# Kernel optimization log

Measured on AMD Instinct MI355X. Metric: run time of the kernel, lower is better.

## Reference

```python
import math
import jax, jax.numpy as jnp
import numpy as np

B, S, D = 8, 2048, 512
D_MODEL = 512

def setup_inputs() -> dict:
    key = jax.random.key(0)
    kq, kk, kv = jax.random.split(key, 3)
    return {
        "query": jax.random.normal(kq, (B, S, D), dtype=jnp.float32),
        "key":   jax.random.normal(kk, (B, S, D), dtype=jnp.float32),
        "value": jax.random.normal(kv, (B, S, D), dtype=jnp.float32),
    }

def reference(query, key, value):
    # scores: [B, S, S]
    scores = jnp.einsum("bqd,bkd->bqk", query, key) / math.sqrt(D_MODEL)
    k = max(1, int(scores.shape[-1] * 0.1))
    top_scores, top_idx = jax.lax.top_k(scores, k)  # [B, S, k]
    # scatter top-k scores into a zero matrix (non-topk entries stay 0,
    # and DO participate in the softmax, matching the torch code)
    b_idx = jnp.arange(scores.shape[0])[:, None, None]
    q_idx = jnp.arange(scores.shape[1])[None, :, None]
    sparse = jnp.zeros_like(scores).at[b_idx, q_idx, top_idx].set(top_scores)
    attn = jax.nn.softmax(sparse, axis=-1)
    return jnp.einsum("bqk,bkd->bqd", attn, value)
```

## Files before the change

kernel.cpp:

```cpp
#include <hip/hip_runtime.h>
#include <math.h>

#define B_ 8
#define S_ 2048
#define D_ 512
#define KTOP 204
#define QK_SCALE 0.044194173824159216f

typedef short bfrag8 __attribute__((ext_vector_type(8)));
typedef float facc4 __attribute__((ext_vector_type(4)));

__device__ __forceinline__ unsigned short f2bf(float f) {
  unsigned u = __float_as_uint(f);
  u += 0x7FFFu + ((u >> 16) & 1);
  return (unsigned short)(u >> 16);
}

__device__ __forceinline__ unsigned fkey(float f) {
  unsigned b = __float_as_uint(f);
  return (b & 0x80000000u) ? ~b : (b | 0x80000000u);
}
__device__ __forceinline__ float keyfloat(unsigned k) {
  unsigned b = (k & 0x80000000u) ? (k & 0x7FFFFFFFu) : ~k;
  return __uint_as_float(b);
}

__device__ __forceinline__ void load16(const unsigned short* g, unsigned short* l) {
  __builtin_amdgcn_global_load_lds(
      (const __attribute__((address_space(1))) void*)g,
      (__attribute__((address_space(3))) void*)l, 16, 0, 0);
}

__global__ __launch_bounds__(256) void cvt_qk(const float* __restrict__ Q,
                                              const float* __restrict__ K,
                                              unsigned short* __restrict__ Qb,
                                              unsigned short* __restrict__ Kb) {
  const float* in = blockIdx.y ? K : Q;
  unsigned short* out = blockIdx.y ? Kb : Qb;
  int i = (blockIdx.x * 256 + threadIdx.x) * 4;
  float4 v = *(const float4*)(in + i);
  ushort4 o;
  o.x = f2bf(v.x); o.y = f2bf(v.y); o.z = f2bf(v.z); o.w = f2bf(v.w);
  *(ushort4*)(out + i) = o;
}

__global__ __launch_bounds__(256) void transpose_v(const float* __restrict__ V,
                                                   unsigned short* __restrict__ VT) {
  __shared__ float tile[32][33];
  int b = blockIdx.z;
  int d0 = blockIdx.x * 32, k0 = blockIdx.y * 32;
  const float* Vb = V + (size_t)b * S_ * D_;
  unsigned short* VTb = VT + (size_t)b * D_ * S_;
  int c = threadIdx.x & 31, r = threadIdx.x >> 5;
#pragma unroll
  for (int rr = 0; rr < 32; rr += 8)
    tile[r + rr][c] = Vb[(size_t)(k0 + r + rr) * D_ + d0 + c];
  __syncthreads();
#pragma unroll
  for (int rr = 0; rr < 32; rr += 8)
    VTb[(size_t)(d0 + r + rr) * S_ + k0 + c] = f2bf(tile[c][r + rr]);
}

__global__ __launch_bounds__(256) void gemm_qk(
    const unsigned short* __restrict__ A, int lda, long long astr,
    const unsigned short* __restrict__ Bm, int ldb, long long bstr,
    float* __restrict__ C, int ldc, long long cstr,
    int kdim, float scale) {
  const unsigned j = blockIdx.x + 16u * blockIdx.y + 256u * blockIdx.z;
  const unsigned bz = j & 7u;
  const unsigned q = j >> 3;
  const unsigned by = q & 15u;
  const unsigned bx = q >> 4;

  __shared__ unsigned short smA[128 * 32];
  __shared__ unsigned short smB[128 * 32];
  const int tid = threadIdx.x;
  const int wave = tid >> 6, lane = tid & 63;
  const int quad = lane >> 4, l15 = lane & 15;
  const unsigned short* Ab = A + (long long)bz * astr + (size_t)(by * 128) * lda;
  const unsigned short* Bb = Bm + (long long)bz * bstr + (size_t)(bx * 128) * ldb;
  const int srow = tid >> 2;
  const int scol = (tid & 3) * 8;
  unsigned short* lA0 = smA + wave * 512;
  unsigned short* lA1 = smA + 2048 + wave * 512;
  unsigned short* lB0 = smB + wave * 512;
  unsigned short* lB1 = smB + 2048 + wave * 512;
  const int mrow = 64 * (wave >> 1);
  const int nrow = 64 * (wave & 1);

  facc4 acc[4][4];
  const facc4 fzero = {0.f, 0.f, 0.f, 0.f};
#pragma unroll
  for (int i = 0; i < 4; ++i)
#pragma unroll
    for (int j2 = 0; j2 < 4; ++j2) acc[i][j2] = fzero;

  for (int k0 = 0; k0 < kdim; k0 += 32) {
    __syncthreads();
    load16(Ab + (size_t)srow * lda + k0 + scol, lA0);
    load16(Ab + (size_t)(srow + 64) * lda + k0 + scol, lA1);
    load16(Bb + (size_t)srow * ldb + k0 + scol, lB0);
    load16(Bb + (size_t)(srow + 64) * ldb + k0 + scol, lB1);
    __syncthreads();
    bfrag8 af[4], bq[4];
#pragma unroll
    for (int i = 0; i < 4; ++i)
      af[i] = *(const bfrag8*)(smA + (mrow + 16 * i + l15) * 32 + quad * 8);
#pragma unroll
    for (int j2 = 0; j2 < 4; ++j2)
      bq[j2] = *(const bfrag8*)(smB + (nrow + 16 * j2 + l15) * 32 + quad * 8);
#pragma unroll
    for (int i = 0; i < 4; ++i)
#pragma unroll
      for (int j2 = 0; j2 < 4; ++j2)
        acc[i][j2] = __builtin_amdgcn_mfma_f32_16x16x32_bf16(af[i], bq[j2], acc[i][j2], 0, 0, 0);
  }

  float* Cb = C + (long long)bz * cstr;
  const int mg = by * 128 + mrow;
  const int ng = bx * 128 + nrow;
#pragma unroll
  for (int i = 0; i < 4; ++i)
#pragma unroll
    for (int j2 = 0; j2 < 4; ++j2)
#pragma unroll
      for (int r = 0; r < 4; ++r)
        Cb[(size_t)(mg + 16 * i + quad * 4 + r) * ldc + ng + 16 * j2 + l15] = acc[i][j2][r] * scale;
}

__global__ __launch_bounds__(256) void gemm_pv(
    const unsigned short* __restrict__ A, int lda, long long astr,
    const unsigned short* __restrict__ Bm, int ldb, long long bstr,
    float* __restrict__ C, int ldc, long long cstr,
    int kdim, float scale) {
  const unsigned j = blockIdx.x + 4u * blockIdx.y + 64u * blockIdx.z;
  const unsigned bz = j & 7u;
  const unsigned q = j >> 3;
  const unsigned bx = q & 3u;
  const unsigned by = q >> 2;

  __shared__ unsigned short smA[128 * 32];
  __shared__ unsigned short smB[128 * 32];
  const int tid = threadIdx.x;
  const int wave = tid >> 6, lane = tid & 63;
  const int quad = lane >> 4, l15 = lane & 15;
  const unsigned short* Ab = A + (long long)bz * astr + (size_t)(by * 128) * lda;
  const unsigned short* Bb = Bm + (long long)bz * bstr + (size_t)(bx * 128) * ldb;
  const int srow = tid >> 2;
  const int scol = (tid & 3) * 8;
  unsigned short* lA0 = smA + wave * 512;
  unsigned short* lA1 = smA + 2048 + wave * 512;
  unsigned short* lB0 = smB + wave * 512;
  unsigned short* lB1 = smB + 2048 + wave * 512;
  const int mrow = 64 * (wave >> 1);
  const int nrow = 64 * (wave & 1);

  facc4 acc[4][4];
  const facc4 fzero = {0.f, 0.f, 0.f, 0.f};
#pragma unroll
  for (int i = 0; i < 4; ++i)
#pragma unroll
    for (int j2 = 0; j2 < 4; ++j2) acc[i][j2] = fzero;

  for (int k0 = 0; k0 < kdim; k0 += 32) {
    __syncthreads();
    load16(Ab + (size_t)srow * lda + k0 + scol, lA0);
    load16(Ab + (size_t)(srow + 64) * lda + k0 + scol, lA1);
    load16(Bb + (size_t)srow * ldb + k0 + scol, lB0);
    load16(Bb + (size_t)(srow + 64) * ldb + k0 + scol, lB1);
    __syncthreads();
    bfrag8 af[4], bq[4];
#pragma unroll
    for (int i = 0; i < 4; ++i)
      af[i] = *(const bfrag8*)(smA + (mrow + 16 * i + l15) * 32 + quad * 8);
#pragma unroll
    for (int j2 = 0; j2 < 4; ++j2)
      bq[j2] = *(const bfrag8*)(smB + (nrow + 16 * j2 + l15) * 32 + quad * 8);
#pragma unroll
    for (int i = 0; i < 4; ++i)
#pragma unroll
      for (int j2 = 0; j2 < 4; ++j2)
        acc[i][j2] = __builtin_amdgcn_mfma_f32_16x16x32_bf16(af[i], bq[j2], acc[i][j2], 0, 0, 0);
  }

  float* Cb = C + (long long)bz * cstr;
  const int mg = by * 128 + mrow;
  const int ng = bx * 128 + nrow;
#pragma unroll
  for (int i = 0; i < 4; ++i)
#pragma unroll
    for (int j2 = 0; j2 < 4; ++j2)
#pragma unroll
      for (int r = 0; r < 4; ++r)
        Cb[(size_t)(mg + 16 * i + quad * 4 + r) * ldc + ng + 16 * j2 + l15] = acc[i][j2][r] * scale;
}

__global__ __launch_bounds__(256) void topk_softmax(float* __restrict__ scores) {
  __shared__ unsigned binsAll[4][256];
  const int tid = threadIdx.x;
  const int wave = tid >> 6, lane = tid & 63;
  const long long row = (long long)blockIdx.x * 4 + wave;
  float* srow = scores + row * 2048;
  unsigned* bins = binsAll[wave];

  unsigned k[32];
#pragma unroll
  for (int c = 0; c < 4; ++c) {
    float4 a = *(const float4*)(srow + c * 512 + lane * 8);
    float4 b = *(const float4*)(srow + c * 512 + lane * 8 + 4);
    k[c * 8 + 0] = fkey(a.x); k[c * 8 + 1] = fkey(a.y);
    k[c * 8 + 2] = fkey(a.z); k[c * 8 + 3] = fkey(a.w);
    k[c * 8 + 4] = fkey(b.x); k[c * 8 + 5] = fkey(b.y);
    k[c * 8 + 6] = fkey(b.z); k[c * 8 + 7] = fkey(b.w);
  }

  unsigned kmax = 0;
#pragma unroll
  for (int i = 0; i < 32; ++i) kmax = max(kmax, k[i]);
#pragma unroll
  for (int off = 1; off < 64; off <<= 1)
    kmax = max(kmax, (unsigned)__shfl_xor((int)kmax, off));
  const float m = fmaxf(keyfloat(kmax), 0.f);

  unsigned prefix = 0, mmask = 0, krem = KTOP;
  for (int shift = 24; shift >= 0; shift -= 8) {
    uint4 z; z.x = z.y = z.z = z.w = 0;
    *(uint4*)(bins + lane * 4) = z;
#pragma unroll
    for (int i = 0; i < 32; ++i)
      if ((k[i] & mmask) == prefix) atomicAdd(&bins[(k[i] >> shift) & 255], 1u);
    uint4 b = *(const uint4*)(bins + lane * 4);
    unsigned s = b.x + b.y + b.z + b.w;
    unsigned t = s;
#pragma unroll
    for (int off = 1; off < 64; off <<= 1) {
      unsigned u = (unsigned)__shfl_down((int)t, off);
      t += (lane + off < 64) ? u : 0u;
    }
    const unsigned texcl = t - s;
    const unsigned c3 = texcl + b.w;
    const unsigned c2 = c3 + b.z;
    const unsigned c1 = c2 + b.y;
    const unsigned c0 = c1 + b.x;
    unsigned pack = 0;
    if (c0 >= krem && c1 < krem)   pack = ((krem - c1) << 8) | (lane * 4 + 0);
    if (c1 >= krem && c2 < krem)   pack = ((krem - c2) << 8) | (lane * 4 + 1);
    if (c2 >= krem && c3 < krem)   pack = ((krem - c3) << 8) | (lane * 4 + 2);
    if (c3 >= krem && texcl < krem) pack = ((krem - texcl) << 8) | (lane * 4 + 3);
#pragma unroll
    for (int off = 1; off < 64; off <<= 1)
      pack |= (unsigned)__shfl_xor((int)pack, off);
    prefix |= (pack & 255u) << shift;
    krem = pack >> 8;
    mmask |= 0xFFu << shift;
  }
  const unsigned tkey = prefix;

  unsigned cut;
  {
    unsigned tiem = 0;
#pragma unroll
    for (int i = 0; i < 32; ++i)
      if (k[i] == tkey) tiem |= 1u << i;
    unsigned need = krem;
    for (;;) {
      unsigned myidx = 0xFFFFFFFFu;
      if (tiem) {
        int i = __ffs((int)tiem) - 1;
        myidx = ((unsigned)(i >> 3)) * 512u + (unsigned)lane * 8u + (unsigned)(i & 7);
      }
      unsigned minidx = myidx;
#pragma unroll
      for (int off = 1; off < 64; off <<= 1)
        minidx = min(minidx, (unsigned)__shfl_xor((int)minidx, off));
      if (--need == 0 || minidx == 0xFFFFFFFFu) { cut = minidx; break; }
      if (myidx == minidx) tiem &= tiem - 1;
    }
  }

  const float eqw = __expf(keyfloat(tkey) - m);
  const float base = __expf(-m);
  float zsum = 0.f;
#pragma unroll
  for (int i = 0; i < 32; ++i) {
    const unsigned key = k[i];
    const unsigned idx = ((unsigned)(i >> 3)) * 512u + (unsigned)lane * 8u + (unsigned)(i & 7);
    float w;
    if (key > tkey) w = __expf(keyfloat(key) - m);
    else w = (key == tkey && idx <= cut) ? eqw : base;
    zsum += w;
    k[i] = __float_as_uint(w);
  }
#pragma unroll
  for (int off = 1; off < 64; off <<= 1) zsum += __shfl_xor(zsum, off);
  const float invZ = 1.f / zsum;

  unsigned short* arow = (unsigned short*)scores + row * 4096;
#pragma unroll
  for (int c = 0; c < 4; ++c) {
    union { unsigned short u[8]; int4 v4; } pk;
#pragma unroll
    for (int j = 0; j < 8; ++j)
      pk.u[j] = f2bf(__uint_as_float(k[c * 8 + j]) * invZ);
    *(int4*)(arow + c * 512 + lane * 8) = pk.v4;
  }
}

extern "C" void kernel_launch(void* const* d_in, const int* in_sizes, int n_in,
                              void* d_out, int out_size, void* d_ws, size_t ws_size,
                              hipStream_t stream) {
  const float* Q = (const float*)d_in[0];
  const float* K = (const float*)d_in[1];
  const float* V = (const float*)d_in[2];
  float* out = (float*)d_out;
  char* ws = (char*)d_ws;
  unsigned short* Qb = (unsigned short*)(ws);
  unsigned short* Kb = (unsigned short*)(ws + ((size_t)16 << 20));
  unsigned short* VT = (unsigned short*)(ws + ((size_t)32 << 20));
  float* scores = (float*)(ws + ((size_t)48 << 20));

  const int nel = B_ * S_ * D_;
  cvt_qk<<<dim3(nel / 1024, 2), 256, 0, stream>>>(Q, K, Qb, Kb);
  transpose_v<<<dim3(D_ / 32, S_ / 32, B_), 256, 0, stream>>>(V, VT);
  gemm_qk<<<dim3(S_ / 128, S_ / 128, B_), 256, 0, stream>>>(
      Qb, D_, (long long)S_ * D_, Kb, D_, (long long)S_ * D_,
      scores, S_, (long long)S_ * S_, D_, QK_SCALE);
  topk_softmax<<<B_ * S_ / 4, 256, 0, stream>>>(scores);
  gemm_pv<<<dim3(D_ / 128, S_ / 128, B_), 256, 0, stream>>>(
      (const unsigned short*)scores, 4096, (long long)S_ * 4096,
      VT, S_, (long long)D_ * S_, out, D_, (long long)S_ * D_, S_, 1.0f);
}
```

Measured before the change: 319.0 us.

## Merge prep kernels and split top-k histogram bins across half-waves

Combines the Q/K bf16 conversion and the V transpose into one launch, which removes a kernel launch boundary. In the top-k softmax, each half-wave now gets its own padded histogram copy, so LDS atomic contention drops at the cost of an extra bin read and add. The original floats are kept in registers so exp can use them directly instead of decoding keys. The bf16 conversion for the common base and tie weights is precomputed. Holding the extra 32 floats per lane raises register pressure.

```diff
diff --git a/kernel.cpp b/kernel.cpp
--- a/kernel.cpp
+++ b/kernel.cpp
@@ -31,34 +31,37 @@
       (__attribute__((address_space(3))) void*)l, 16, 0, 0);
 }
 
-__global__ __launch_bounds__(256) void cvt_qk(const float* __restrict__ Q,
-                                              const float* __restrict__ K,
-                                              unsigned short* __restrict__ Qb,
-                                              unsigned short* __restrict__ Kb) {
-  const float* in = blockIdx.y ? K : Q;
-  unsigned short* out = blockIdx.y ? Kb : Qb;
-  int i = (blockIdx.x * 256 + threadIdx.x) * 4;
-  float4 v = *(const float4*)(in + i);
-  ushort4 o;
-  o.x = f2bf(v.x); o.y = f2bf(v.y); o.z = f2bf(v.z); o.w = f2bf(v.w);
-  *(ushort4*)(out + i) = o;
-}
-
-__global__ __launch_bounds__(256) void transpose_v(const float* __restrict__ V,
-                                                   unsigned short* __restrict__ VT) {
+__global__ __launch_bounds__(256) void prep(const float* __restrict__ Q,
+                                            const float* __restrict__ K,
+                                            const float* __restrict__ V,
+                                            unsigned short* __restrict__ Qb,
+                                            unsigned short* __restrict__ Kb,
+                                            unsigned short* __restrict__ VT) {
   __shared__ float tile[32][33];
-  int b = blockIdx.z;
-  int d0 = blockIdx.x * 32, k0 = blockIdx.y * 32;
-  const float* Vb = V + (size_t)b * S_ * D_;
-  unsigned short* VTb = VT + (size_t)b * D_ * S_;
-  int c = threadIdx.x & 31, r = threadIdx.x >> 5;
-#pragma unroll
-  for (int rr = 0; rr < 32; rr += 8)
-    tile[r + rr][c] = Vb[(size_t)(k0 + r + rr) * D_ + d0 + c];
-  __syncthreads();
-#pragma unroll
-  for (int rr = 0; rr < 32; rr += 8)
-    VTb[(size_t)(d0 + r + rr) * S_ + k0 + c] = f2bf(tile[c][r + rr]);
+  const unsigned j = blockIdx.x;
+  if (j < 16384u) {
+    const float* in = (j < 8192u) ? Q : K;
+    unsigned short* out = (j < 8192u) ? Qb : Kb;
+    int i = (int)(((j & 8191u) * 256u + threadIdx.x) * 4u);
+    float4 v = *(const float4*)(in + i);
+    ushort4 o;
+    o.x = f2bf(v.x); o.y = f2bf(v.y); o.z = f2bf(v.z); o.w = f2bf(v.w);
+    *(ushort4*)(out + i) = o;
+  } else {
+    const unsigned t = j - 16384u;
+    const int d0 = (int)(t & 15u) * 32, k0 = (int)((t >> 4) & 63u) * 32;
+    const int b = (int)(t >> 10);
+    const float* Vb = V + (size_t)b * S_ * D_;
+    unsigned short* VTb = VT + (size_t)b * D_ * S_;
+    int c = threadIdx.x & 31, r = threadIdx.x >> 5;
+#pragma unroll
+    for (int rr = 0; rr < 32; rr += 8)
+      tile[r + rr][c] = Vb[(size_t)(k0 + r + rr) * D_ + d0 + c];
+    __syncthreads();
+#pragma unroll
+    for (int rr = 0; rr < 32; rr += 8)
+      VTb[(size_t)(d0 + r + rr) * S_ + k0 + c] = f2bf(tile[c][r + rr]);
+  }
 }
 
 __global__ __launch_bounds__(256) void gemm_qk(
@@ -196,23 +199,25 @@
 }
 
 __global__ __launch_bounds__(256) void topk_softmax(float* __restrict__ scores) {
-  __shared__ unsigned binsAll[4][256];
+  __shared__ unsigned binsAll[4][544];
   const int tid = threadIdx.x;
   const int wave = tid >> 6, lane = tid & 63;
   const long long row = (long long)blockIdx.x * 4 + wave;
   float* srow = scores + row * 2048;
   unsigned* bins = binsAll[wave];
-
+  const unsigned gb = (unsigned)(lane >> 5) * 272u;
+
+  float fv[32];
   unsigned k[32];
 #pragma unroll
   for (int c = 0; c < 4; ++c) {
     float4 a = *(const float4*)(srow + c * 512 + lane * 8);
     float4 b = *(const float4*)(srow + c * 512 + lane * 8 + 4);
-    k[c * 8 + 0] = fkey(a.x); k[c * 8 + 1] = fkey(a.y);
-    k[c * 8 + 2] = fkey(a.z); k[c * 8 + 3] = fkey(a.w);
-    k[c * 8 + 4] = fkey(b.x); k[c * 8 + 5] = fkey(b.y);
-    k[c * 8 + 6] = fkey(b.z); k[c * 8 + 7] = fkey(b.w);
-  }
+    fv[c * 8 + 0] = a.x; fv[c * 8 + 1] = a.y; fv[c * 8 + 2] = a.z; fv[c * 8 + 3] = a.w;
+    fv[c * 8 + 4] = b.x; fv[c * 8 + 5] = b.y; fv[c * 8 + 6] = b.z; fv[c * 8 + 7] = b.w;
+  }
+#pragma unroll
+  for (int i = 0; i < 32; ++i) k[i] = fkey(fv[i]);
 
   unsigned kmax = 0;
 #pragma unroll
@@ -225,11 +230,17 @@
   unsigned prefix = 0, mmask = 0, krem = KTOP;
   for (int shift = 24; shift >= 0; shift -= 8) {
     uint4 z; z.x = z.y = z.z = z.w = 0;
-    *(uint4*)(bins + lane * 4) = z;
+    *(uint4*)(bins + lane * 8) = z;
+    *(uint4*)(bins + lane * 8 + 4) = z;
+    if (lane < 8) *(uint4*)(bins + 512 + lane * 4) = z;
 #pragma unroll
     for (int i = 0; i < 32; ++i)
-      if ((k[i] & mmask) == prefix) atomicAdd(&bins[(k[i] >> shift) & 255], 1u);
-    uint4 b = *(const uint4*)(bins + lane * 4);
+      if ((k[i] & mmask) == prefix)
+        atomicAdd(&bins[gb + ((k[i] >> shift) & 255u)], 1u);
+    uint4 b0 = *(const uint4*)(bins + lane * 4);
+    uint4 b1 = *(const uint4*)(bins + 272 + lane * 4);
+    uint4 b;
+    b.x = b0.x + b1.x; b.y = b0.y + b1.y; b.z = b0.z + b1.z; b.w = b0.w + b1.w;
     unsigned s = b.x + b.y + b.z + b.w;
     unsigned t = s;
 #pragma unroll
@@ -286,7 +297,7 @@
     const unsigned key = k[i];
     const unsigned idx = ((unsigned)(i >> 3)) * 512u + (unsigned)lane * 8u + (unsigned)(i & 7);
     float w;
-    if (key > tkey) w = __expf(keyfloat(key) - m);
+    if (key > tkey) w = __expf(fv[i] - m);
     else w = (key == tkey && idx <= cut) ? eqw : base;
     zsum += w;
     k[i] = __float_as_uint(w);
@@ -295,13 +306,21 @@
   for (int off = 1; off < 64; off <<= 1) zsum += __shfl_xor(zsum, off);
   const float invZ = 1.f / zsum;
 
+  const unsigned ubase = __float_as_uint(base);
+  const unsigned ueqw = __float_as_uint(eqw);
+  const unsigned short bf_base = f2bf(base * invZ);
+  const unsigned short bf_eq = f2bf(eqw * invZ);
   unsigned short* arow = (unsigned short*)scores + row * 4096;
 #pragma unroll
   for (int c = 0; c < 4; ++c) {
     union { unsigned short u[8]; int4 v4; } pk;
 #pragma unroll
-    for (int j = 0; j < 8; ++j)
-      pk.u[j] = f2bf(__uint_as_float(k[c * 8 + j]) * invZ);
+    for (int j = 0; j < 8; ++j) {
+      const unsigned wb = k[c * 8 + j];
+      pk.u[j] = (wb == ubase) ? bf_base
+              : (wb == ueqw)  ? bf_eq
+              : f2bf(__uint_as_float(wb) * invZ);
+    }
     *(int4*)(arow + c * 512 + lane * 8) = pk.v4;
   }
 }
@@ -319,9 +338,7 @@
   unsigned short* VT = (unsigned short*)(ws + ((size_t)32 << 20));
   float* scores = (float*)(ws + ((size_t)48 << 20));
 
-  const int nel = B_ * S_ * D_;
-  cvt_qk<<<dim3(nel / 1024, 2), 256, 0, stream>>>(Q, K, Qb, Kb);
-  transpose_v<<<dim3(D_ / 32, S_ / 32, B_), 256, 0, stream>>>(V, VT);
+  prep<<<24576, 256, 0, stream>>>(Q, K, V, Qb, Kb, VT);
   gemm_qk<<<dim3(S_ / 128, S_ / 128, B_), 256, 0, stream>>>(
       Qb, D_, (long long)S_ * D_, Kb, D_, (long long)S_ * D_,
       scores, S_, (long long)S_ * S_, D_, QK_SCALE);
```

Measured after the change: 326.5 us. 1.02x slower.
